# Kernel optimization log

Measured on AMD Instinct MI355X. Metric: run time of the kernel, lower is better.

## Reference

```python
import jax, jax.numpy as jnp
import numpy as np

N_HEADS = 32
N_KV_HEADS = 8
HEAD_DIM = 128
GROUP = N_HEADS // N_KV_HEADS  # 4
MAX_SEQ_LEN = 4096
DIM = 3072
NEG_BIG = 1.0e9


def setup_inputs() -> dict:
    key = jax.random.key(0)
    ks = jax.random.split(key, 8)
    B, T = 1, 2048
    return {
        "x": jax.random.normal(ks[0], (B, T, DIM), dtype=jnp.float32),
        "freqs_cos": jax.random.uniform(ks[1], (T, HEAD_DIM // 2), dtype=jnp.float32),
        "freqs_sin": jax.random.uniform(ks[2], (T, HEAD_DIM // 2), dtype=jnp.float32),
        "input_pos": jnp.arange(T, dtype=jnp.int32),
        "wq": jax.random.normal(ks[3], (N_HEADS * HEAD_DIM, DIM), dtype=jnp.float32) * 0.02,
        "wk": jax.random.normal(ks[4], (N_KV_HEADS * HEAD_DIM, DIM), dtype=jnp.float32) * 0.02,
        "wv": jax.random.normal(ks[5], (N_KV_HEADS * HEAD_DIM, DIM), dtype=jnp.float32) * 0.02,
        "wo": jax.random.normal(ks[6], (DIM, N_HEADS * HEAD_DIM), dtype=jnp.float32) * 0.02,
        "k_cache": jnp.zeros((1, N_KV_HEADS, MAX_SEQ_LEN, HEAD_DIM), dtype=jnp.float32),
        "v_cache": jnp.zeros((1, N_KV_HEADS, MAX_SEQ_LEN, HEAD_DIM), dtype=jnp.float32),
    }


def _rotate_half(x):
    half = x.shape[-1] // 2
    return jnp.concatenate([-x[..., half:], x[..., :half]], axis=-1)


def _apply_rope(q, k, freqs_cos, freqs_sin):
    # freqs: [T, D/2] -> [1, T, 1, D] (tiled x2, matching torch repeat on last dim)
    fc = jnp.concatenate([freqs_cos, freqs_cos], axis=-1)[None, :, None, :]
    fs = jnp.concatenate([freqs_sin, freqs_sin], axis=-1)[None, :, None, :]
    qf = q.astype(jnp.float32)
    kf = k.astype(jnp.float32)
    q_out = qf * fc + _rotate_half(qf) * fs
    k_out = kf * fc + _rotate_half(kf) * fs
    return q_out.astype(q.dtype), k_out.astype(k.dtype)


def reference(x, freqs_cos, freqs_sin, input_pos, wq, wk, wv, wo, k_cache, v_cache):
    B, T, _ = x.shape
    # QKV projections
    q = (x @ wq.T).reshape(B, T, N_HEADS, HEAD_DIM)
    k = (x @ wk.T).reshape(B, T, N_KV_HEADS, HEAD_DIM)
    v = (x @ wv.T).reshape(B, T, N_KV_HEADS, HEAD_DIM)
    # split-half RoPE (computed in fp32)
    q, k = _apply_rope(q, k, freqs_cos, freqs_sin)
    # StaticKVCache.update: scatter [B,H,T,D] into [1,H,S,D] cache at input_pos (dim 2)
    kc = k_cache.at[:, :, input_pos].set(k.transpose(0, 2, 1, 3))
    vc = v_cache.at[:, :, input_pos].set(v.transpose(0, 2, 1, 3))
    # MetalSDPA: additive causal mask over full cache length
    S = kc.shape[2]
    k_pos = jnp.arange(S)
    valid = jnp.clip(input_pos[:, None] - k_pos[None, :] + 1, 0, 1)  # [T, S]
    mask = (valid.astype(q.dtype) - 1.0) * NEG_BIG
    # GQA attention: group q heads per kv head
    qg = q.transpose(0, 2, 1, 3).reshape(B, N_KV_HEADS, GROUP, T, HEAD_DIM)
    scale = 1.0 / jnp.sqrt(jnp.asarray(HEAD_DIM, dtype=q.dtype))
    scores = jnp.einsum('bhgtd,bhsd->bhgts', qg, kc) * scale + mask  # [B,Hk,G,T,S]
    attn = jax.nn.softmax(scores, axis=-1)
    y = jnp.einsum('bhgts,bhsd->bhgtd', attn, vc)
    y = y.reshape(B, N_HEADS, T, HEAD_DIM).transpose(0, 2, 1, 3).reshape(B, T, N_HEADS * HEAD_DIM)
    return y @ wo.T
```

## Files before the change

### kernel.cpp

```cpp
#include <hip/hip_runtime.h>

typedef __attribute__((ext_vector_type(8))) short bf16x8;
typedef __attribute__((ext_vector_type(4))) float f32x4;

#define T_SEQ   2048
#define DIM     3072
#define NQH     32
#define NKVH    8
#define HD      128
#define QDIM    4096
#define KVDIM   1024
#define QKVDIM  6144

#define AS1 __attribute__((address_space(1)))
#define AS3 __attribute__((address_space(3)))

static __device__ __forceinline__ unsigned short f2bf(float f) {
  unsigned u = __float_as_uint(f);
  u += 0x7FFFu + ((u >> 16) & 1u);
  return (unsigned short)(u >> 16);
}
static __device__ __forceinline__ float bf2f(unsigned short h) {
  return __uint_as_float(((unsigned)h) << 16);
}
static __device__ __forceinline__ unsigned pkbf(float lo, float hi) {
  unsigned r;
  asm("v_cvt_pk_bf16_f32 %0, %1, %2" : "=v"(r) : "v"(lo), "v"(hi));
  return r;
}

static __device__ __forceinline__ void gload_lds16(const unsigned short* g, unsigned short* l) {
  __builtin_amdgcn_global_load_lds((AS1 void*)(g), (AS3 void*)(l), 16, 0, 0);
}

__global__ void cvt_all(const float* __restrict__ x,  const float* __restrict__ wq,
                        const float* __restrict__ wk, const float* __restrict__ wv,
                        const float* __restrict__ wo,
                        unsigned short* __restrict__ xb,
                        unsigned short* __restrict__ wqkvb,
                        unsigned short* __restrict__ wob) {
  const int N0 = 1572864;
  const int E1 = N0 + 3145728;
  const int E2 = E1 + 786432;
  const int E3 = E2 + 786432;
  const int E4 = E3 + 3145728;
  const int stride = gridDim.x * blockDim.x;
  for (int i = blockIdx.x * blockDim.x + threadIdx.x; i < E4; i += stride) {
    const float* s; unsigned short* d; int off;
    if (i < N0)      { s = x;  d = xb;               off = i; }
    else if (i < E1) { s = wq; d = wqkvb;            off = i - N0; }
    else if (i < E2) { s = wk; d = wqkvb + 12582912; off = i - E1; }
    else if (i < E3) { s = wv; d = wqkvb + 15728640; off = i - E2; }
    else             { s = wo; d = wob;              off = i - E3; }
    float4 v = reinterpret_cast<const float4*>(s)[off];
    ushort4 o;
    o.x = f2bf(v.x); o.y = f2bf(v.y); o.z = f2bf(v.z); o.w = f2bf(v.w);
    reinterpret_cast<ushort4*>(d + (size_t)off * 4)[0] = o;
  }
}

template<int OUTBF>
__global__ __launch_bounds__(256) void gemm_bt(
    const unsigned short* __restrict__ A, const unsigned short* __restrict__ B,
    float* __restrict__ Cf, unsigned short* __restrict__ Cb,
    int M, int N, int K) {
  __shared__ unsigned short la[128 * 64];
  __shared__ unsigned short lb[128 * 64];
  const int nbx = N >> 7;
  const int q8 = gridDim.x >> 3;
  int bid = blockIdx.x;
  bid = (bid & 7) * q8 + (bid >> 3);
  const int bx = bid % nbx, by = bid / nbx;
  const int tid = threadIdx.x;
  const int ln = tid & 63;
  const int wave = tid >> 6;
  const int lr = ln & 15, lg = ln >> 4;
  const int wr = wave >> 1, wc = wave & 1;
  const int rowA0 = by << 7, rowB0 = bx << 7;

  f32x4 acc[4][4] = {};

  const int ktn = K >> 6;
  for (int kt = 0; kt < ktn; kt++) {
    __syncthreads();
#pragma unroll
    for (int it = 0; it < 4; it++) {
      int ci = it * 256 + tid;
      int r = ci >> 3, cpos = ci & 7;
      int c = cpos ^ (r & 7);
      const unsigned short* gA = A + (size_t)(rowA0 + r) * K + kt * 64 + c * 8;
      const unsigned short* gB = B + (size_t)(rowB0 + r) * K + kt * 64 + c * 8;
      gload_lds16(gA, &la[ci * 8]);
      gload_lds16(gB, &lb[ci * 8]);
    }
    __syncthreads();
#pragma unroll
    for (int kk = 0; kk < 2; kk++) {
      bf16x8 af[4], bfr[4];
#pragma unroll
      for (int mi = 0; mi < 4; mi++) {
        int r = wr * 64 + mi * 16 + lr;
        int p = (kk * 4 + lg) ^ (r & 7);
        af[mi] = *reinterpret_cast<const bf16x8*>(&la[r * 64 + p * 8]);
      }
#pragma unroll
      for (int ni = 0; ni < 4; ni++) {
        int r = wc * 64 + ni * 16 + lr;
        int p = (kk * 4 + lg) ^ (r & 7);
        bfr[ni] = *reinterpret_cast<const bf16x8*>(&lb[r * 64 + p * 8]);
      }
#pragma unroll
      for (int mi = 0; mi < 4; mi++)
#pragma unroll
        for (int ni = 0; ni < 4; ni++)
          acc[mi][ni] = __builtin_amdgcn_mfma_f32_16x16x32_bf16(af[mi], bfr[ni], acc[mi][ni], 0, 0, 0);
    }
  }
#pragma unroll
  for (int mi = 0; mi < 4; mi++)
#pragma unroll
    for (int ni = 0; ni < 4; ni++)
#pragma unroll
      for (int j = 0; j < 4; j++) {
        int r = rowA0 + wr * 64 + mi * 16 + lg * 4 + j;
        int cc = rowB0 + wc * 64 + ni * 16 + lr;
        if (OUTBF) Cb[(size_t)r * N + cc] = f2bf(acc[mi][ni][j]);
        else       Cf[(size_t)r * N + cc] = acc[mi][ni][j];
      }
}

__global__ void rope_repack(const unsigned short* __restrict__ qkv,
                            const float* __restrict__ fc, const float* __restrict__ fs,
                            unsigned short* __restrict__ qo, unsigned short* __restrict__ ko) {
  int idx = blockIdx.x * blockDim.x + threadIdx.x;
  int d = idx & 63;
  int hh = (idx >> 6) % 40;
  int t = idx / 2560;
  const unsigned short* src = qkv + (size_t)t * QKVDIM + hh * 128;
  float x0 = bf2f(src[d]);
  float x1 = bf2f(src[d + 64]);
  float c = fc[t * 64 + d], s = fs[t * 64 + d];
  float o0 = x0 * c - x1 * s;
  float o1 = x1 * c + x0 * s;
  if (hh < 32) {
    unsigned short* dst = qo + (size_t)t * QDIM + hh * 128;
    dst[d] = f2bf(o0); dst[d + 64] = f2bf(o1);
  } else {
    unsigned short* dst = ko + (size_t)t * KVDIM + (hh - 32) * 128;
    dst[d] = f2bf(o0); dst[d + 64] = f2bf(o1);
  }
}

__global__ void vtrans(const unsigned short* __restrict__ qkv, unsigned short* __restrict__ vt) {
  __shared__ unsigned short tile[64][68];
  int tb = blockIdx.x * 64, cb = blockIdx.y * 64;
  int tid = threadIdx.x;
#pragma unroll
  for (int i = 0; i < 16; i++) {
    int e = i * 256 + tid;
    int tl = e >> 6, cl = e & 63;
    tile[tl][cl] = qkv[(size_t)(tb + tl) * QKVDIM + 5120 + cb + cl];
  }
  __syncthreads();
#pragma unroll
  for (int i = 0; i < 16; i++) {
    int e = i * 256 + tid;
    int cl = e >> 6, tl = e & 63;
    vt[(size_t)(cb + cl) * T_SEQ + tb + tl] = tile[tl][cl];
  }
}

__global__ __launch_bounds__(256) void attn_fwd(
    const unsigned short* __restrict__ q, const unsigned short* __restrict__ k,
    const unsigned short* __restrict__ vt, unsigned short* __restrict__ y) {
  __shared__ unsigned short k_lds[2][32 * 128];
  __shared__ unsigned short v_lds[2][128 * 32];
  __shared__ unsigned short p_lds[4][16 * 40];
  __shared__ float a_lds[4][16];
  const int tid = threadIdx.x;
  const int ln = tid & 63;
  const int wave = tid >> 6;
  const int lr = ln & 15, lg = ln >> 4;

  const int kh = blockIdx.x & 7;
  const int i = blockIdx.x >> 3;
  const int qh = i & 3;
  const int pr = i >> 2;
  const int qta = pr, qtb = 31 - pr;
  const int h = kh * 4 + qh;

  const int qra0 = qta * 64 + wave * 16, qrowa = qra0 + lr;
  const int qrb0 = qtb * 64 + wave * 16, qrowb = qrb0 + lr;
  const float SL2E = 0.08838834764831845f * 1.44269504088896f;
  const float NEGINF = -__builtin_inff();

  bf16x8 qfa[4], qfb[4];
  {
    const unsigned short* qba = q + (size_t)qrowa * QDIM + h * HD + lg * 8;
    const unsigned short* qbb = q + (size_t)qrowb * QDIM + h * HD + lg * 8;
#pragma unroll
    for (int dc = 0; dc < 4; dc++) {
      qfa[dc] = *reinterpret_cast<const bf16x8*>(qba + dc * 32);
      qfb[dc] = *reinterpret_cast<const bf16x8*>(qbb + dc * 32);
    }
  }

  f32x4 acca[8] = {}, accb[8] = {};
  float ma = NEGINF, la = 0.f, mb = NEGINF, lb = 0.f;

  const int krow0 = tid >> 4,  kcol0 = tid & 15;
  const int krow1 = 16 + krow0;
  const int vrow0 = tid >> 2,  vcol0 = tid & 3;
  const int vrow1 = 64 + vrow0;

  auto tile_compute = [&](int sb, int cur, const bf16x8 (&qf)[4], f32x4 (&acc)[8],
                          float& m, float& lsum, int qr0, int qrow) {
    f32x4 s0t = {0.f, 0.f, 0.f, 0.f}, s1t = {0.f, 0.f, 0.f, 0.f};
    __builtin_amdgcn_s_setprio(1);
#pragma unroll
    for (int dc = 0; dc < 4; dc++) {
      int c = lg + dc * 4;
      int p = c ^ (lr & 7);
      bf16x8 a0 = *reinterpret_cast<const bf16x8*>(&k_lds[cur][lr * 128 + p * 8]);
      bf16x8 a1 = *reinterpret_cast<const bf16x8*>(&k_lds[cur][(lr + 16) * 128 + p * 8]);
      s0t = __builtin_amdgcn_mfma_f32_16x16x32_bf16(a0, qf[dc], s0t, 0, 0, 0);
      s1t = __builtin_amdgcn_mfma_f32_16x16x32_bf16(a1, qf[dc], s1t, 0, 0, 0);
    }
    __builtin_amdgcn_s_setprio(0);

    float vv[8];
    if (sb + 31 <= qr0) {
#pragma unroll
      for (int jj = 0; jj < 4; jj++) { vv[jj] = s0t[jj]; vv[jj + 4] = s1t[jj]; }
    } else {
      const int base0 = sb + lg * 4;
#pragma unroll
      for (int jj = 0; jj < 4; jj++) {
        vv[jj]     = (base0 + jj      <= qrow) ? s0t[jj] : NEGINF;
        vv[jj + 4] = (base0 + jj + 16 <= qrow) ? s1t[jj] : NEGINF;
      }
    }

    float mx = fmaxf(fmaxf(fmaxf(vv[0], vv[1]), fmaxf(vv[2], vv[3])),
                     fmaxf(fmaxf(vv[4], vv[5]), fmaxf(vv[6], vv[7])));
    mx = fmaxf(mx, __shfl_xor(mx, 16));
    mx = fmaxf(mx, __shfl_xor(mx, 32));

    const bool doresc = __any(mx > m + 60.0f);
    const float mn = doresc ? fmaxf(m, mx) : m;

    float p[8], ps = 0.f;
#pragma unroll
    for (int ii = 0; ii < 8; ii++) { p[ii] = exp2f((vv[ii] - mn) * SL2E); ps += p[ii]; }
    ps += __shfl_xor(ps, 16);
    ps += __shfl_xor(ps, 32);

    uint2 w0, w1;
    w0.x = pkbf(p[0], p[1]); w0.y = pkbf(p[2], p[3]);
    w1.x = pkbf(p[4], p[5]); w1.y = pkbf(p[6], p[7]);
    *reinterpret_cast<uint2*>(&p_lds[wave][lr * 40 + lg * 4])      = w0;
    *reinterpret_cast<uint2*>(&p_lds[wave][lr * 40 + 16 + lg * 4]) = w1;

    if (doresc) {
      const float alpha = exp2f((m - mn) * SL2E);
      lsum = lsum * alpha + ps;
      m = mn;
      a_lds[wave][lr] = alpha;
      asm volatile("s_waitcnt lgkmcnt(0)" ::: "memory");
      float4 a4 = *reinterpret_cast<const float4*>(&a_lds[wave][lg * 4]);
#pragma unroll
      for (int dc2 = 0; dc2 < 8; dc2++) {
        acc[dc2][0] *= a4.x; acc[dc2][1] *= a4.y;
        acc[dc2][2] *= a4.z; acc[dc2][3] *= a4.w;
      }
    } else {
      lsum += ps;
      asm volatile("s_waitcnt lgkmcnt(0)" ::: "memory");
    }

    bf16x8 pa = *reinterpret_cast<const bf16x8*>(&p_lds[wave][lr * 40 + lg * 8]);
    __builtin_amdgcn_s_setprio(1);
#pragma unroll
    for (int dc2 = 0; dc2 < 8; dc2++) {
      int d = dc2 * 16 + lr;
      int p2 = lg ^ ((d >> 1) & 3);
      bf16x8 bv = *reinterpret_cast<const bf16x8*>(&v_lds[cur][d * 32 + p2 * 8]);
      acc[dc2] = __builtin_amdgcn_mfma_f32_16x16x32_bf16(pa, bv, acc[dc2], 0, 0, 0);
    }
    __builtin_amdgcn_s_setprio(0);
  };

  const int ntiles = (qtb * 64 + 95) >> 5;

  {
    bf16x8 kr0 = *reinterpret_cast<const bf16x8*>(k + (size_t)krow0 * KVDIM + kh * HD + kcol0 * 8);
    bf16x8 kr1 = *reinterpret_cast<const bf16x8*>(k + (size_t)krow1 * KVDIM + kh * HD + kcol0 * 8);
    bf16x8 vr0 = *reinterpret_cast<const bf16x8*>(vt + (size_t)(kh * HD + vrow0) * T_SEQ + vcol0 * 8);
    bf16x8 vr1 = *reinterpret_cast<const bf16x8*>(vt + (size_t)(kh * HD + vrow1) * T_SEQ + vcol0 * 8);
    *reinterpret_cast<bf16x8*>(&k_lds[0][krow0 * 128 + (kcol0 ^ (krow0 & 7)) * 8]) = kr0;
    *reinterpret_cast<bf16x8*>(&k_lds[0][krow1 * 128 + (kcol0 ^ (krow1 & 7)) * 8]) = kr1;
    *reinterpret_cast<bf16x8*>(&v_lds[0][vrow0 * 32 + (vcol0 ^ ((vrow0 >> 1) & 3)) * 8]) = vr0;
    *reinterpret_cast<bf16x8*>(&v_lds[0][vrow1 * 32 + (vcol0 ^ ((vrow1 >> 1) & 3)) * 8]) = vr1;
  }
  __syncthreads();

  for (int st = 0; st < ntiles; st++) {
    const int sb = st * 32;
    const int cur = st & 1;
    const bool more = (st + 1 < ntiles);

    bf16x8 kr0, kr1, vr0, vr1;
    if (more) {
      const int sb1 = sb + 32;
      kr0 = *reinterpret_cast<const bf16x8*>(k + (size_t)(sb1 + krow0) * KVDIM + kh * HD + kcol0 * 8);
      kr1 = *reinterpret_cast<const bf16x8*>(k + (size_t)(sb1 + krow1) * KVDIM + kh * HD + kcol0 * 8);
      vr0 = *reinterpret_cast<const bf16x8*>(vt + (size_t)(kh * HD + vrow0) * T_SEQ + sb1 + vcol0 * 8);
      vr1 = *reinterpret_cast<const bf16x8*>(vt + (size_t)(kh * HD + vrow1) * T_SEQ + sb1 + vcol0 * 8);
    }

    if (sb <= qrb0 + 15) tile_compute(sb, cur, qfb, accb, mb, lb, qrb0, qrowb);
    if (sb <= qra0 + 15) tile_compute(sb, cur, qfa, acca, ma, la, qra0, qrowa);

    if (more) {
      const int nxt = cur ^ 1;
      *reinterpret_cast<bf16x8*>(&k_lds[nxt][krow0 * 128 + (kcol0 ^ (krow0 & 7)) * 8]) = kr0;
      *reinterpret_cast<bf16x8*>(&k_lds[nxt][krow1 * 128 + (kcol0 ^ (krow1 & 7)) * 8]) = kr1;
      *reinterpret_cast<bf16x8*>(&v_lds[nxt][vrow0 * 32 + (vcol0 ^ ((vrow0 >> 1) & 3)) * 8]) = vr0;
      *reinterpret_cast<bf16x8*>(&v_lds[nxt][vrow1 * 32 + (vcol0 ^ ((vrow1 >> 1) & 3)) * 8]) = vr1;
      __syncthreads();
    }
  }

  a_lds[wave][lr] = 1.0f / lb;
  asm volatile("s_waitcnt lgkmcnt(0)" ::: "memory");
  float4 l4 = *reinterpret_cast<const float4*>(&a_lds[wave][lg * 4]);
  {
    float li[4] = {l4.x, l4.y, l4.z, l4.w};
#pragma unroll
    for (int jj = 0; jj < 4; jj++) {
      int r = qrb0 + lg * 4 + jj;
#pragma unroll
      for (int dc2 = 0; dc2 < 8; dc2++)
        y[(size_t)r * QDIM + h * HD + dc2 * 16 + lr] = f2bf(accb[dc2][jj] * li[jj]);
    }
  }
  a_lds[wave][lr] = 1.0f / la;
  asm volatile("s_waitcnt lgkmcnt(0)" ::: "memory");
  l4 = *reinterpret_cast<const float4*>(&a_lds[wave][lg * 4]);
  {
    float li[4] = {l4.x, l4.y, l4.z, l4.w};
#pragma unroll
    for (int jj = 0; jj < 4; jj++) {
      int r = qra0 + lg * 4 + jj;
#pragma unroll
      for (int dc2 = 0; dc2 < 8; dc2++)
        y[(size_t)r * QDIM + h * HD + dc2 * 16 + lr] = f2bf(acca[dc2][jj] * li[jj]);
    }
  }
}

extern "C" void kernel_launch(void* const* d_in, const int* in_sizes, int n_in,
                              void* d_out, int out_size, void* d_ws, size_t ws_size,
                              hipStream_t stream) {
  (void)in_sizes; (void)n_in; (void)out_size; (void)ws_size;
  const float* x    = (const float*)d_in[0];
  const float* fcos = (const float*)d_in[1];
  const float* fsin = (const float*)d_in[2];
  const float* wq   = (const float*)d_in[4];
  const float* wk   = (const float*)d_in[5];
  const float* wv   = (const float*)d_in[6];
  const float* wo   = (const float*)d_in[7];
  float* out = (float*)d_out;
  char* ws = (char*)d_ws;

  unsigned short* x_bf    = (unsigned short*)(ws);
  unsigned short* wqkv_bf = (unsigned short*)(ws + 12582912);
  unsigned short* qkv_bf  = (unsigned short*)(ws + 50331648);
  unsigned short* q_bf    = (unsigned short*)(ws);
  unsigned short* k_bf    = (unsigned short*)(ws + 16777216);
  unsigned short* vt_bf   = (unsigned short*)(ws + 20971520);
  unsigned short* y_bf    = (unsigned short*)(ws + 25165824);
  unsigned short* wo_bf   = (unsigned short*)(ws + 75497472);

  cvt_all<<<4096, 256, 0, stream>>>(x, wq, wk, wv, wo, x_bf, wqkv_bf, wo_bf);
  gemm_bt<1><<<768, 256, 0, stream>>>(x_bf, wqkv_bf, nullptr, qkv_bf, 2048, 6144, 3072);

  rope_repack<<<20480, 256, 0, stream>>>(qkv_bf, fcos, fsin, q_bf, k_bf);
  vtrans<<<dim3(32, 16), 256, 0, stream>>>(qkv_bf, vt_bf);

  attn_fwd<<<512, 256, 0, stream>>>(q_bf, k_bf, vt_bf, y_bf);
  gemm_bt<0><<<384, 256, 0, stream>>>(y_bf, wo_bf, out, nullptr, 2048, 3072, 4096);
}
```

Baseline: 319.8 us.

## Fuse RoPE and V transpose into QKV GEMM epilogue, overlap wo conversion with attention

The QKV projection GEMM now uses full-width 128-column tiles per wave, so each block covers one whole head. Its epilogue applies split-half RoPE directly for Q/K heads and writes V transposed through LDS, which removes the separate rope_repack and vtrans kernels and the intermediate QKV buffer round trip. The fp32-to-bf16 conversion of wo moves out of cvt_all into 256 extra blocks of the attention launch, so it runs alongside attention. The cost is a different wave tiling in the QKV GEMM (2x8 fragments, all waves reading all of B), which changes LDS traffic and register pressure, and attention blocks now share the GPU with conversion blocks.

```diff
diff --git a/kernel.cpp b/kernel.cpp
--- a/kernel.cpp
+++ b/kernel.cpp
@@ -10,7 +10,6 @@
 #define HD      128
 #define QDIM    4096
 #define KVDIM   1024
-#define QKVDIM  6144
 
 #define AS1 __attribute__((address_space(1)))
 #define AS3 __attribute__((address_space(3)))
@@ -35,23 +34,19 @@
 
 __global__ void cvt_all(const float* __restrict__ x,  const float* __restrict__ wq,
                         const float* __restrict__ wk, const float* __restrict__ wv,
-                        const float* __restrict__ wo,
                         unsigned short* __restrict__ xb,
-                        unsigned short* __restrict__ wqkvb,
-                        unsigned short* __restrict__ wob) {
+                        unsigned short* __restrict__ wqkvb) {
   const int N0 = 1572864;
   const int E1 = N0 + 3145728;
   const int E2 = E1 + 786432;
   const int E3 = E2 + 786432;
-  const int E4 = E3 + 3145728;
   const int stride = gridDim.x * blockDim.x;
-  for (int i = blockIdx.x * blockDim.x + threadIdx.x; i < E4; i += stride) {
+  for (int i = blockIdx.x * blockDim.x + threadIdx.x; i < E3; i += stride) {
     const float* s; unsigned short* d; int off;
     if (i < N0)      { s = x;  d = xb;               off = i; }
     else if (i < E1) { s = wq; d = wqkvb;            off = i - N0; }
     else if (i < E2) { s = wk; d = wqkvb + 12582912; off = i - E1; }
-    else if (i < E3) { s = wv; d = wqkvb + 15728640; off = i - E2; }
-    else             { s = wo; d = wob;              off = i - E3; }
+    else             { s = wv; d = wqkvb + 15728640; off = i - E2; }
     float4 v = reinterpret_cast<const float4*>(s)[off];
     ushort4 o;
     o.x = f2bf(v.x); o.y = f2bf(v.y); o.z = f2bf(v.z); o.w = f2bf(v.w);
@@ -59,11 +54,110 @@
   }
 }
 
-template<int OUTBF>
+__global__ __launch_bounds__(256) void gemm_qkv(
+    const unsigned short* __restrict__ A, const unsigned short* __restrict__ B,
+    const float* __restrict__ fc, const float* __restrict__ fs,
+    unsigned short* __restrict__ qo, unsigned short* __restrict__ ko,
+    unsigned short* __restrict__ vt) {
+  __shared__ unsigned short epi[128 * 132];
+  unsigned short* la = epi;
+  unsigned short* lb = epi + 8192;
+  const int K = DIM, nbx = 48;
+  const int q8 = gridDim.x >> 3;
+  int bid = blockIdx.x;
+  bid = (bid & 7) * q8 + (bid >> 3);
+  const int bx = bid % nbx, by = bid / nbx;
+  const int tid = threadIdx.x;
+  const int ln = tid & 63;
+  const int wave = tid >> 6;
+  const int lr = ln & 15, lg = ln >> 4;
+  const int rowA0 = by << 7, rowB0 = bx << 7;
+
+  f32x4 acc[2][8] = {};
+
+  const int ktn = K >> 6;
+  for (int kt = 0; kt < ktn; kt++) {
+    __syncthreads();
+#pragma unroll
+    for (int it = 0; it < 4; it++) {
+      int ci = it * 256 + tid;
+      int r = ci >> 3, cpos = ci & 7;
+      int c = cpos ^ (r & 7);
+      gload_lds16(A + (size_t)(rowA0 + r) * K + kt * 64 + c * 8, &la[ci * 8]);
+      gload_lds16(B + (size_t)(rowB0 + r) * K + kt * 64 + c * 8, &lb[ci * 8]);
+    }
+    __syncthreads();
+#pragma unroll
+    for (int kk = 0; kk < 2; kk++) {
+      bf16x8 af_[2], bf_[8];
+#pragma unroll
+      for (int mi = 0; mi < 2; mi++) {
+        int r = wave * 32 + mi * 16 + lr;
+        int p = (kk * 4 + lg) ^ (r & 7);
+        af_[mi] = *reinterpret_cast<const bf16x8*>(&la[r * 64 + p * 8]);
+      }
+#pragma unroll
+      for (int ni = 0; ni < 8; ni++) {
+        int r = ni * 16 + lr;
+        int p = (kk * 4 + lg) ^ (r & 7);
+        bf_[ni] = *reinterpret_cast<const bf16x8*>(&lb[r * 64 + p * 8]);
+      }
+#pragma unroll
+      for (int mi = 0; mi < 2; mi++)
+#pragma unroll
+        for (int ni = 0; ni < 8; ni++)
+          acc[mi][ni] = __builtin_amdgcn_mfma_f32_16x16x32_bf16(af_[mi], bf_[ni], acc[mi][ni], 0, 0, 0);
+    }
+  }
+
+  if (bx < 40) {
+    unsigned short* dst; int dstride;
+    if (bx < 32) { dst = qo + (size_t)bx * 128; dstride = QDIM; }
+    else         { dst = ko + (size_t)(bx - 32) * 128; dstride = KVDIM; }
+#pragma unroll
+    for (int mi = 0; mi < 2; mi++)
+#pragma unroll
+      for (int j = 0; j < 4; j++) {
+        int t = rowA0 + wave * 32 + mi * 16 + lg * 4 + j;
+#pragma unroll
+        for (int ni = 0; ni < 4; ni++) {
+          int d = ni * 16 + lr;
+          float c = fc[t * 64 + d], s = fs[t * 64 + d];
+          float x0 = acc[mi][ni][j], x1 = acc[mi][ni + 4][j];
+          dst[(size_t)t * dstride + d]      = f2bf(x0 * c - x1 * s);
+          dst[(size_t)t * dstride + d + 64] = f2bf(x1 * c + x0 * s);
+        }
+      }
+  } else {
+    __syncthreads();
+#pragma unroll
+    for (int mi = 0; mi < 2; mi++)
+#pragma unroll
+      for (int ni = 0; ni < 8; ni++)
+#pragma unroll
+        for (int j = 0; j < 4; j++) {
+          int r = wave * 32 + mi * 16 + lg * 4 + j;
+          int cc = ni * 16 + lr;
+          epi[r * 132 + cc] = f2bf(acc[mi][ni][j]);
+        }
+    __syncthreads();
+    const int ccol = tid >> 1, th = tid & 1;
+    size_t vrow = (size_t)((bx - 40) * 128 + ccol) * T_SEQ + rowA0 + th * 64;
+#pragma unroll
+    for (int i = 0; i < 16; i++) {
+      ushort4 o;
+      o.x = epi[(th * 64 + i * 4 + 0) * 132 + ccol];
+      o.y = epi[(th * 64 + i * 4 + 1) * 132 + ccol];
+      o.z = epi[(th * 64 + i * 4 + 2) * 132 + ccol];
+      o.w = epi[(th * 64 + i * 4 + 3) * 132 + ccol];
+      *reinterpret_cast<ushort4*>(&vt[vrow + i * 4]) = o;
+    }
+  }
+}
+
 __global__ __launch_bounds__(256) void gemm_bt(
     const unsigned short* __restrict__ A, const unsigned short* __restrict__ B,
-    float* __restrict__ Cf, unsigned short* __restrict__ Cb,
-    int M, int N, int K) {
+    float* __restrict__ Cf, int M, int N, int K) {
   __shared__ unsigned short la[128 * 64];
   __shared__ unsigned short lb[128 * 64];
   const int nbx = N >> 7;
@@ -88,10 +182,8 @@
       int ci = it * 256 + tid;
       int r = ci >> 3, cpos = ci & 7;
       int c = cpos ^ (r & 7);
-      const unsigned short* gA = A + (size_t)(rowA0 + r) * K + kt * 64 + c * 8;
-      const unsigned short* gB = B + (size_t)(rowB0 + r) * K + kt * 64 + c * 8;
-      gload_lds16(gA, &la[ci * 8]);
-      gload_lds16(gB, &lb[ci * 8]);
+      gload_lds16(A + (size_t)(rowA0 + r) * K + kt * 64 + c * 8, &la[ci * 8]);
+      gload_lds16(B + (size_t)(rowB0 + r) * K + kt * 64 + c * 8, &lb[ci * 8]);
     }
     __syncthreads();
 #pragma unroll
@@ -124,55 +216,24 @@
       for (int j = 0; j < 4; j++) {
         int r = rowA0 + wr * 64 + mi * 16 + lg * 4 + j;
         int cc = rowB0 + wc * 64 + ni * 16 + lr;
-        if (OUTBF) Cb[(size_t)r * N + cc] = f2bf(acc[mi][ni][j]);
-        else       Cf[(size_t)r * N + cc] = acc[mi][ni][j];
-      }
-}
-
-__global__ void rope_repack(const unsigned short* __restrict__ qkv,
-                            const float* __restrict__ fc, const float* __restrict__ fs,
-                            unsigned short* __restrict__ qo, unsigned short* __restrict__ ko) {
-  int idx = blockIdx.x * blockDim.x + threadIdx.x;
-  int d = idx & 63;
-  int hh = (idx >> 6) % 40;
-  int t = idx / 2560;
-  const unsigned short* src = qkv + (size_t)t * QKVDIM + hh * 128;
-  float x0 = bf2f(src[d]);
-  float x1 = bf2f(src[d + 64]);
-  float c = fc[t * 64 + d], s = fs[t * 64 + d];
-  float o0 = x0 * c - x1 * s;
-  float o1 = x1 * c + x0 * s;
-  if (hh < 32) {
-    unsigned short* dst = qo + (size_t)t * QDIM + hh * 128;
-    dst[d] = f2bf(o0); dst[d + 64] = f2bf(o1);
-  } else {
-    unsigned short* dst = ko + (size_t)t * KVDIM + (hh - 32) * 128;
-    dst[d] = f2bf(o0); dst[d + 64] = f2bf(o1);
-  }
-}
-
-__global__ void vtrans(const unsigned short* __restrict__ qkv, unsigned short* __restrict__ vt) {
-  __shared__ unsigned short tile[64][68];
-  int tb = blockIdx.x * 64, cb = blockIdx.y * 64;
-  int tid = threadIdx.x;
-#pragma unroll
-  for (int i = 0; i < 16; i++) {
-    int e = i * 256 + tid;
-    int tl = e >> 6, cl = e & 63;
-    tile[tl][cl] = qkv[(size_t)(tb + tl) * QKVDIM + 5120 + cb + cl];
-  }
-  __syncthreads();
-#pragma unroll
-  for (int i = 0; i < 16; i++) {
-    int e = i * 256 + tid;
-    int cl = e >> 6, tl = e & 63;
-    vt[(size_t)(cb + cl) * T_SEQ + tb + tl] = tile[tl][cl];
-  }
+        Cf[(size_t)r * N + cc] = acc[mi][ni][j];
+      }
 }
 
 __global__ __launch_bounds__(256) void attn_fwd(
     const unsigned short* __restrict__ q, const unsigned short* __restrict__ k,
-    const unsigned short* __restrict__ vt, unsigned short* __restrict__ y) {
+    const unsigned short* __restrict__ vt, unsigned short* __restrict__ y,
+    const float* __restrict__ wo, unsigned short* __restrict__ wob) {
+  if (blockIdx.x >= 512) {
+    const int total = 3145728;
+    for (int i = (blockIdx.x - 512) * 256 + threadIdx.x; i < total; i += 65536) {
+      float4 v = reinterpret_cast<const float4*>(wo)[i];
+      ushort4 o;
+      o.x = f2bf(v.x); o.y = f2bf(v.y); o.z = f2bf(v.z); o.w = f2bf(v.w);
+      reinterpret_cast<ushort4*>(wob + (size_t)i * 4)[0] = o;
+    }
+    return;
+  }
   __shared__ unsigned short k_lds[2][32 * 128];
   __shared__ unsigned short v_lds[2][128 * 32];
   __shared__ unsigned short p_lds[4][16 * 40];
@@ -375,19 +436,16 @@
 
   unsigned short* x_bf    = (unsigned short*)(ws);
   unsigned short* wqkv_bf = (unsigned short*)(ws + 12582912);
-  unsigned short* qkv_bf  = (unsigned short*)(ws + 50331648);
-  unsigned short* q_bf    = (unsigned short*)(ws);
-  unsigned short* k_bf    = (unsigned short*)(ws + 16777216);
-  unsigned short* vt_bf   = (unsigned short*)(ws + 20971520);
-  unsigned short* y_bf    = (unsigned short*)(ws + 25165824);
-  unsigned short* wo_bf   = (unsigned short*)(ws + 75497472);
-
-  cvt_all<<<4096, 256, 0, stream>>>(x, wq, wk, wv, wo, x_bf, wqkv_bf, wo_bf);
-  gemm_bt<1><<<768, 256, 0, stream>>>(x_bf, wqkv_bf, nullptr, qkv_bf, 2048, 6144, 3072);
-
-  rope_repack<<<20480, 256, 0, stream>>>(qkv_bf, fcos, fsin, q_bf, k_bf);
-  vtrans<<<dim3(32, 16), 256, 0, stream>>>(qkv_bf, vt_bf);
-
-  attn_fwd<<<512, 256, 0, stream>>>(q_bf, k_bf, vt_bf, y_bf);
-  gemm_bt<0><<<384, 256, 0, stream>>>(y_bf, wo_bf, out, nullptr, 2048, 3072, 4096);
-}
+  unsigned short* q_bf    = (unsigned short*)(ws + 50331648);
+  unsigned short* k_bf    = (unsigned short*)(ws + 67108864);
+  unsigned short* vt_bf   = (unsigned short*)(ws + 71303168);
+  unsigned short* y_bf    = (unsigned short*)(ws + 75497472);
+  unsigned short* wo_bf   = (unsigned short*)(ws);
+
+  cvt_all<<<4096, 256, 0, stream>>>(x, wq, wk, wv, x_bf, wqkv_bf);
+  gemm_qkv<<<768, 256, 0, stream>>>(x_bf, wqkv_bf, fcos, fsin, q_bf, k_bf, vt_bf);
+
+  attn_fwd<<<768, 256, 0, stream>>>(q_bf, k_bf, vt_bf, y_bf, wo, wo_bf);
+
+  gemm_bt<<<384, 256, 0, stream>>>(y_bf, wo_bf, out, 2048, 3072, 4096);
+}
```

Result: slower. 388.9 us (+21.6%).
